# Kernel optimization log

Measured on AMD Instinct MI355X. Metric: run time of the kernel, lower is better.

Reference implementation:

```python
import jax, jax.numpy as jnp
import numpy as np

M, K, N, G = 64, 4096, 11008, 128  # tokens, infeatures, outfeatures, group_size
NUM_GROUPS = K // G  # 32


def _fp8_round_trip(w):
    # Simulate FP8 E4M3 storage of the quantized weight codes.
    return w.astype(jnp.float8_e4m3fn).astype(jnp.float32)


def setup_inputs() -> dict:
    key = jax.random.key(0)
    k1, k2, k3, k4 = jax.random.split(key, 4)
    x = jax.random.normal(k1, (M, K), dtype=jnp.float32)
    # FP8-representable weight codes (post round-trip, stored as f32 values)
    weight = _fp8_round_trip(jax.random.normal(k2, (N, K), dtype=jnp.float32) * 2.0)
    # Per-(out_feature, group) dequant scales, strictly positive
    weight_scale = jax.random.uniform(k3, (N, NUM_GROUPS), dtype=jnp.float32,
                                      minval=0.005, maxval=0.02)
    bias = jax.random.normal(k4, (N,), dtype=jnp.float32)
    return {"x": x, "weight": weight, "weight_scale": weight_scale, "bias": bias}


def reference(x, weight, weight_scale, bias):
    # Dequantize: each group of `G` consecutive in-features of an output row
    # shares one scale -> w_deq[o, i] = weight[o, i] * scale[o, i // G]
    n, k = weight.shape
    g = k // weight_scale.shape[1]
    w_deq = (weight.reshape(n, -1, g) * weight_scale[:, :, None]).reshape(n, k)
    # Fused dequant-matmul: out[m, o] = sum_i x[m, i] * w_deq[o, i] + bias[o]
    out = jnp.einsum("mk,nk->mn", x, w_deq) + bias
    return out
```

## Files before the change

kernel.cpp:

```cpp
#include <hip/hip_runtime.h>


#define Md 64
#define Kd 4096
#define Nd 11008
#define NGROUPS 32
#define BN 64
#define BK 64
#define KSPLIT 8
#define KCHUNK (Kd / KSPLIT)
#define NITER (KCHUNK / BK)
#define NGRP (KCHUNK / 128)
#define XLD (BK + 8)

typedef __attribute__((ext_vector_type(8))) __bf16 bf16x8;
typedef __attribute__((ext_vector_type(4))) float f32x4;

__global__ __launch_bounds__(256, 4)
void qlinear_pass1(const float* __restrict__ x,
                   const float* __restrict__ w,
                   const float* __restrict__ scale,
                   float* __restrict__ ws)
{
    const int tid  = threadIdx.x;
    const int wv   = tid >> 6;
    const int lane = tid & 63;
    const int quad = lane >> 4;
    const int ln   = lane & 15;

    const int n0 = blockIdx.x * BN;
    const int ky = blockIdx.y;
    const int k0 = ky * KCHUNK;

    const int nrow = n0 + wv * 16 + ln;
    const float* wp = w + (size_t)nrow * Kd + k0 + quad * 8;

    const int xrow = tid >> 2;
    const int xc0  = (tid & 3) * 16;
    const float* xp = x + (size_t)xrow * Kd + k0 + xc0;

    __shared__ __bf16 lds_x[Md * XLD];

    float4 sc4 = *(const float4*)(scale + (size_t)nrow * NGROUPS + ky * NGRP);
    const float sc[4] = {sc4.x, sc4.y, sc4.z, sc4.w};

    f32x4 acc[4];
    #pragma unroll
    for (int t = 0; t < 4; ++t) acc[t] = (f32x4){0.f, 0.f, 0.f, 0.f};

    float4 wreg[2][4], xreg[2][4];
    #pragma unroll
    for (int j = 0; j < 4; ++j)
        xreg[0][j] = *(const float4*)(xp + j * 4);
    wreg[0][0] = *(const float4*)(wp + 0);
    wreg[0][1] = *(const float4*)(wp + 4);
    wreg[0][2] = *(const float4*)(wp + 32);
    wreg[0][3] = *(const float4*)(wp + 36);

    #pragma unroll
    for (int g = 0; g < NGRP; ++g) {
        f32x4 pg[4];
        #pragma unroll
        for (int t = 0; t < 4; ++t) pg[t] = (f32x4){0.f, 0.f, 0.f, 0.f};

        #pragma unroll
        for (int sub = 0; sub < 2; ++sub) {
            const int i   = g * 2 + sub;
            const int buf = i & 1;

            #pragma unroll
            for (int j = 0; j < 2; ++j) {
                float4 a = xreg[buf][2 * j], b = xreg[buf][2 * j + 1];
                bf16x8 v = {(__bf16)a.x, (__bf16)a.y, (__bf16)a.z, (__bf16)a.w,
                            (__bf16)b.x, (__bf16)b.y, (__bf16)b.z, (__bf16)b.w};
                *(bf16x8*)&lds_x[xrow * XLD + xc0 + j * 8] = v;
            }
            __syncthreads();

            if (i + 1 < NITER) {
                const int nb = buf ^ 1;
                #pragma unroll
                for (int j = 0; j < 4; ++j)
                    xreg[nb][j] = *(const float4*)(xp + (i + 1) * BK + j * 4);
                wreg[nb][0] = *(const float4*)(wp + (i + 1) * BK + 0);
                wreg[nb][1] = *(const float4*)(wp + (i + 1) * BK + 4);
                wreg[nb][2] = *(const float4*)(wp + (i + 1) * BK + 32);
                wreg[nb][3] = *(const float4*)(wp + (i + 1) * BK + 36);
            }

            #pragma unroll
            for (int ks = 0; ks < 2; ++ks) {
                float4 wa = wreg[buf][2 * ks], wb = wreg[buf][2 * ks + 1];
                bf16x8 wf = {(__bf16)wa.x, (__bf16)wa.y, (__bf16)wa.z, (__bf16)wa.w,
                             (__bf16)wb.x, (__bf16)wb.y, (__bf16)wb.z, (__bf16)wb.w};
                #pragma unroll
                for (int t = 0; t < 4; ++t) {
                    bf16x8 xf = *(const bf16x8*)
                        &lds_x[(t * 16 + ln) * XLD + ks * 32 + quad * 8];
                    pg[t] = __builtin_amdgcn_mfma_f32_16x16x32_bf16(xf, wf, pg[t],
                                                                    0, 0, 0);
                }
            }
            __syncthreads();
        }

        const float s = sc[g];
        #pragma unroll
        for (int t = 0; t < 4; ++t)
            #pragma unroll
            for (int r = 0; r < 4; ++r)
                acc[t][r] += s * pg[t][r];
    }

    float* op = ws + ((size_t)ky * Md) * Nd + n0 + wv * 16 + ln;
    #pragma unroll
    for (int t = 0; t < 4; ++t)
        #pragma unroll
        for (int r = 0; r < 4; ++r)
            op[(size_t)(t * 16 + quad * 4 + r) * Nd] = acc[t][r];
}

__global__ __launch_bounds__(256)
void qlinear_reduce(const float* __restrict__ ws,
                    const float* __restrict__ bias,
                    float* __restrict__ out)
{
    const int idx = blockIdx.x * 256 + threadIdx.x;
    if (idx >= Md * Nd) return;
    const int n = idx % Nd;
    float v = bias[n];
    #pragma unroll
    for (int ky = 0; ky < KSPLIT; ++ky)
        v += ws[(size_t)ky * Md * Nd + idx];
    out[idx] = v;
}

extern "C" void kernel_launch(void* const* d_in, const int* in_sizes, int n_in,
                              void* d_out, int out_size, void* d_ws, size_t ws_size,
                              hipStream_t stream) {
    const float* x     = (const float*)d_in[0];
    const float* w     = (const float*)d_in[1];
    const float* scale = (const float*)d_in[2];
    const float* bias  = (const float*)d_in[3];
    float* out = (float*)d_out;
    float* ws  = (float*)d_ws;

    dim3 grid1(Nd / BN, KSPLIT);
    qlinear_pass1<<<grid1, 256, 0, stream>>>(x, w, scale, ws);

    const int total = Md * Nd;
    qlinear_reduce<<<(total + 255) / 256, 256, 0, stream>>>(ws, bias, out);
}
```

Measured before the change: 274.8 us.

## Stage whole x chunk in LDS once, drop per-step barriers, raise K split

Raises the K split from 8 to 16. Each block now converts its whole 256-wide x chunk to bf16 into LDS up front, in a k-group-major layout, behind a single barrier. The main loop then streams weights through a 3-deep register ring with no per-iteration __syncthreads, which removes barrier stalls and the interleaved x conversion. It also vectorises the reduce kernel to float4. The cost is twice the partial-sum workspace traffic in the reduce step, plus a larger grid with more blocks.

```diff
diff --git a/kernel.cpp b/kernel.cpp
--- a/kernel.cpp
+++ b/kernel.cpp
@@ -6,12 +6,11 @@
 #define Nd 11008
 #define NGROUPS 32
 #define BN 64
-#define BK 64
-#define KSPLIT 8
+#define KSPLIT 16
 #define KCHUNK (Kd / KSPLIT)
-#define NITER (KCHUNK / BK)
+#define NSTEP (KCHUNK / 32)
 #define NGRP (KCHUNK / 128)
-#define XLD (BK + 8)
+#define KGS 64
 
 typedef __attribute__((ext_vector_type(8))) __bf16 bf16x8;
 typedef __attribute__((ext_vector_type(4))) float f32x4;
@@ -32,30 +31,46 @@
     const int ky = blockIdx.y;
     const int k0 = ky * KCHUNK;
 
+    __shared__ __bf16 lds_x[(KCHUNK / 8) * 64 * 8];
+
+    {
+        const int m = tid >> 2;
+        const int q = tid & 3;
+        const float* xp = x + (size_t)m * Kd + k0;
+        #pragma unroll
+        for (int j = 0; j < 4; ++j) {
+            const int c = q * 16 + j * 64;
+            float4 a = *(const float4*)(xp + c);
+            float4 b = *(const float4*)(xp + c + 4);
+            float4 e = *(const float4*)(xp + c + 8);
+            float4 d = *(const float4*)(xp + c + 12);
+            bf16x8 v0 = {(__bf16)a.x, (__bf16)a.y, (__bf16)a.z, (__bf16)a.w,
+                         (__bf16)b.x, (__bf16)b.y, (__bf16)b.z, (__bf16)b.w};
+            bf16x8 v1 = {(__bf16)e.x, (__bf16)e.y, (__bf16)e.z, (__bf16)e.w,
+                         (__bf16)d.x, (__bf16)d.y, (__bf16)d.z, (__bf16)d.w};
+            const int kg = c >> 3;
+            *(bf16x8*)&lds_x[(size_t)(kg * KGS + m) * 8]       = v0;
+            *(bf16x8*)&lds_x[(size_t)((kg + 1) * KGS + m) * 8] = v1;
+        }
+    }
+    __syncthreads();
+
     const int nrow = n0 + wv * 16 + ln;
     const float* wp = w + (size_t)nrow * Kd + k0 + quad * 8;
 
-    const int xrow = tid >> 2;
-    const int xc0  = (tid & 3) * 16;
-    const float* xp = x + (size_t)xrow * Kd + k0 + xc0;
-
-    __shared__ __bf16 lds_x[Md * XLD];
-
-    float4 sc4 = *(const float4*)(scale + (size_t)nrow * NGROUPS + ky * NGRP);
-    const float sc[4] = {sc4.x, sc4.y, sc4.z, sc4.w};
+    const float2 sc2 = *(const float2*)(scale + (size_t)nrow * NGROUPS
+                                        + ky * NGRP);
+    const float sc[2] = {sc2.x, sc2.y};
 
     f32x4 acc[4];
     #pragma unroll
     for (int t = 0; t < 4; ++t) acc[t] = (f32x4){0.f, 0.f, 0.f, 0.f};
 
-    float4 wreg[2][4], xreg[2][4];
-    #pragma unroll
-    for (int j = 0; j < 4; ++j)
-        xreg[0][j] = *(const float4*)(xp + j * 4);
-    wreg[0][0] = *(const float4*)(wp + 0);
-    wreg[0][1] = *(const float4*)(wp + 4);
-    wreg[0][2] = *(const float4*)(wp + 32);
-    wreg[0][3] = *(const float4*)(wp + 36);
+    float4 wb[3][2];
+    wb[0][0] = *(const float4*)(wp + 0);
+    wb[0][1] = *(const float4*)(wp + 4);
+    wb[1][0] = *(const float4*)(wp + 32);
+    wb[1][1] = *(const float4*)(wp + 36);
 
     #pragma unroll
     for (int g = 0; g < NGRP; ++g) {
@@ -64,44 +79,23 @@
         for (int t = 0; t < 4; ++t) pg[t] = (f32x4){0.f, 0.f, 0.f, 0.f};
 
         #pragma unroll
-        for (int sub = 0; sub < 2; ++sub) {
-            const int i   = g * 2 + sub;
-            const int buf = i & 1;
-
+        for (int ks = 0; ks < 4; ++ks) {
+            const int step = g * 4 + ks;
+            if (step + 2 < NSTEP) {
+                const int s = step + 2;
+                wb[s % 3][0] = *(const float4*)(wp + s * 32);
+                wb[s % 3][1] = *(const float4*)(wp + s * 32 + 4);
+            }
+            float4 wa = wb[step % 3][0], wbv = wb[step % 3][1];
+            bf16x8 wf = {(__bf16)wa.x,  (__bf16)wa.y,  (__bf16)wa.z,  (__bf16)wa.w,
+                         (__bf16)wbv.x, (__bf16)wbv.y, (__bf16)wbv.z, (__bf16)wbv.w};
             #pragma unroll
-            for (int j = 0; j < 2; ++j) {
-                float4 a = xreg[buf][2 * j], b = xreg[buf][2 * j + 1];
-                bf16x8 v = {(__bf16)a.x, (__bf16)a.y, (__bf16)a.z, (__bf16)a.w,
-                            (__bf16)b.x, (__bf16)b.y, (__bf16)b.z, (__bf16)b.w};
-                *(bf16x8*)&lds_x[xrow * XLD + xc0 + j * 8] = v;
+            for (int t = 0; t < 4; ++t) {
+                bf16x8 xf = *(const bf16x8*)
+                    &lds_x[(size_t)((step * 4 + quad) * KGS + t * 16 + ln) * 8];
+                pg[t] = __builtin_amdgcn_mfma_f32_16x16x32_bf16(xf, wf, pg[t],
+                                                                0, 0, 0);
             }
-            __syncthreads();
-
-            if (i + 1 < NITER) {
-                const int nb = buf ^ 1;
-                #pragma unroll
-                for (int j = 0; j < 4; ++j)
-                    xreg[nb][j] = *(const float4*)(xp + (i + 1) * BK + j * 4);
-                wreg[nb][0] = *(const float4*)(wp + (i + 1) * BK + 0);
-                wreg[nb][1] = *(const float4*)(wp + (i + 1) * BK + 4);
-                wreg[nb][2] = *(const float4*)(wp + (i + 1) * BK + 32);
-                wreg[nb][3] = *(const float4*)(wp + (i + 1) * BK + 36);
-            }
-
-            #pragma unroll
-            for (int ks = 0; ks < 2; ++ks) {
-                float4 wa = wreg[buf][2 * ks], wb = wreg[buf][2 * ks + 1];
-                bf16x8 wf = {(__bf16)wa.x, (__bf16)wa.y, (__bf16)wa.z, (__bf16)wa.w,
-                             (__bf16)wb.x, (__bf16)wb.y, (__bf16)wb.z, (__bf16)wb.w};
-                #pragma unroll
-                for (int t = 0; t < 4; ++t) {
-                    bf16x8 xf = *(const bf16x8*)
-                        &lds_x[(t * 16 + ln) * XLD + ks * 32 + quad * 8];
-                    pg[t] = __builtin_amdgcn_mfma_f32_16x16x32_bf16(xf, wf, pg[t],
-                                                                    0, 0, 0);
-                }
-            }
-            __syncthreads();
         }
 
         const float s = sc[g];
@@ -125,14 +119,16 @@
                     const float* __restrict__ bias,
                     float* __restrict__ out)
 {
-    const int idx = blockIdx.x * 256 + threadIdx.x;
-    if (idx >= Md * Nd) return;
-    const int n = idx % Nd;
-    float v = bias[n];
+    const int idx4 = blockIdx.x * 256 + threadIdx.x;
+    if (idx4 >= Md * Nd / 4) return;
+    const int n4 = idx4 % (Nd / 4);
+    float4 v = *(const float4*)(bias + n4 * 4);
     #pragma unroll
-    for (int ky = 0; ky < KSPLIT; ++ky)
-        v += ws[(size_t)ky * Md * Nd + idx];
-    out[idx] = v;
+    for (int ky = 0; ky < KSPLIT; ++ky) {
+        float4 p = *(const float4*)(ws + (size_t)ky * Md * Nd + (size_t)idx4 * 4);
+        v.x += p.x; v.y += p.y; v.z += p.z; v.w += p.w;
+    }
+    *(float4*)(out + (size_t)idx4 * 4) = v;
 }
 
 extern "C" void kernel_launch(void* const* d_in, const int* in_sizes, int n_in,
@@ -148,6 +144,6 @@
     dim3 grid1(Nd / BN, KSPLIT);
     qlinear_pass1<<<grid1, 256, 0, stream>>>(x, w, scale, ws);
 
-    const int total = Md * Nd;
-    qlinear_reduce<<<(total + 255) / 256, 256, 0, stream>>>(ws, bias, out);
+    const int total4 = Md * Nd / 4;
+    qlinear_reduce<<<(total4 + 255) / 256, 256, 0, stream>>>(ws, bias, out);
 }
```

New measurement: 278.5 us. Within noise of the previous version (+1.3%).
